# Kernel tuning notes

Measured on AMD Instinct MI355X. Metric: run time of the kernel, lower is better.

Reference implementation:

```python
import jax, jax.numpy as jnp
import numpy as np

KH, KW = 7, 7      # t2t kernel_size
ST = 3             # stride
PD = 3             # padding
K = KH * KW        # 49 taps per patch


def _patch_indices(H, W):
    """Linear indices into the padded (Hp,Wp) image for every (patch l, tap k)."""
    Hp, Wp = H + 2 * PD, W + 2 * PD
    oh = (H + 2 * PD - KH) // ST + 1
    ow = (W + 2 * PD - KW) // ST + 1
    ki, kj = np.meshgrid(np.arange(KH), np.arange(KW), indexing='ij')
    rows = (np.arange(oh) * ST)[:, None, None, None] + ki[None, None]   # (oh,1,kh,kw)
    cols = (np.arange(ow) * ST)[None, :, None, None] + kj[None, None]   # (1,ow,kh,kw)
    idx = (rows * Wp + cols).reshape(oh * ow, K)                        # (L, 49)
    return jnp.asarray(idx), Hp, Wp, oh * ow


def setup_inputs() -> dict:
    key = jax.random.key(0)
    k1, k2, k3 = jax.random.split(key, 3)
    b, n, d, hd = 2, 5760, 512, 1960
    return {
        'x': jax.random.normal(k1, (b, n, d), dtype=jnp.float32),
        'W1': jax.random.normal(k2, (d, hd), dtype=jnp.float32) * 0.02,
        'b1': jnp.zeros((hd,), dtype=jnp.float32),
        'W2': jax.random.normal(k3, (hd, d), dtype=jnp.float32) * 0.02,
        'b2': jnp.zeros((d,), dtype=jnp.float32),
        'out_h': 60,
        'out_w': 108,
    }


def reference(x, W1, b1, W2, b2, out_h, out_w):
    H, W = int(out_h), int(out_w)
    idx, Hp, Wp, L = _patch_indices(H, W)          # idx: (L, 49)
    idxf = idx.reshape(-1)                         # (L*49,)

    b, n, _ = x.shape
    h = x @ W1 + b1                                # (b, n, 1960)
    hd = h.shape[-1]
    C = hd // K                                    # 40 fold channels
    Bp = (b * n) // L                              # fold batch (= b * t)

    # fold input layout: (Bp, C, K, L) -> scatter-add into padded image
    patches = h.reshape(Bp, L, C, K)
    vals = jnp.transpose(patches, (0, 2, 1, 3)).reshape(Bp * C, L * K)
    img = jnp.zeros((Bp * C, Hp * Wp), x.dtype).at[:, idxf].add(vals)

    # overlap-count normalizer (fold of ones), same for every batch/channel
    count = jnp.zeros((Hp * Wp,), x.dtype).at[idxf].add(jnp.ones_like(idxf, x.dtype))

    # crop padding (as F.fold does), normalize, re-pad with zeros (as F.unfold does)
    img = img.reshape(Bp, C, Hp, Wp)[:, :, PD:PD + H, PD:PD + W]
    cnt = count.reshape(Hp, Wp)[PD:PD + H, PD:PD + W]
    img = img / cnt
    flat = jnp.pad(img, ((0, 0), (0, 0), (PD, PD), (PD, PD))).reshape(Bp * C, Hp * Wp)

    # unfold: gather the same taps back, restore (b, n, hd) token layout
    g = flat[:, idxf].reshape(Bp, C, L, K)
    g = jnp.transpose(g, (0, 2, 1, 3)).reshape(b, n, hd)

    return jax.nn.gelu(g, approximate=False) @ W2 + b2
```

## Files before the change

### kernel.cpp

```cpp
#include <hip/hip_runtime.h>

typedef _Float16 f16;
typedef __attribute__((ext_vector_type(8))) _Float16 half8;
typedef __attribute__((ext_vector_type(4))) _Float16 half4;
typedef __attribute__((ext_vector_type(4))) float f32x4;

#define LDS_AS __attribute__((address_space(3)))
#define GLB_AS __attribute__((address_space(1)))

__device__ __forceinline__ void load16_lds(const f16* g, f16* l) {
    __builtin_amdgcn_global_load_lds((GLB_AS void*)(g), (LDS_AS void*)(l), 16, 0, 0);
}

__global__ __launch_bounds__(256, 2) void gemm1(
    const f16* __restrict__ A, const f16* __restrict__ Bt,
    const float* __restrict__ bias, f16* __restrict__ C)
{
    const int id  = blockIdx.x;
    const int xcd = id & 7;
    const int r   = id >> 3;
    const int mt  = r & 15;
    const int nt  = xcd + 8 * (r >> 4);
    if (nt >= 90) return;
    const int m0 = mt * 128, n0 = nt * 128;
    const int K = 512, ldc = 11520;

    __shared__ f16 As[128 * 32];
    __shared__ f16 Bs[128 * 32];
    const int tid  = threadIdx.x;
    const int wave = tid >> 6;
    const int lane = tid & 63;

    const int s0 = tid, s1 = tid + 256;
    const f16* gA0 = A  + (m0 + (s0 >> 2)) * K + (s0 & 3) * 8;
    const f16* gA1 = A  + (m0 + (s1 >> 2)) * K + (s1 & 3) * 8;
    const f16* gB0 = Bt + (n0 + (s0 >> 2)) * K + (s0 & 3) * 8;
    const f16* gB1 = Bt + (n0 + (s1 >> 2)) * K + (s1 & 3) * 8;
    f16* lA0 = &As[wave * 512];
    f16* lA1 = &As[2048 + wave * 512];
    f16* lB0 = &Bs[wave * 512];
    f16* lB1 = &Bs[2048 + wave * 512];

    const int wm = (wave >> 1) * 64;
    const int wn = (wave & 1) * 64;
    const int lr = lane & 15;
    const int k8 = (lane >> 4) * 8;

    f32x4 acc[4][4];
#pragma unroll
    for (int i = 0; i < 4; ++i)
#pragma unroll
        for (int j = 0; j < 4; ++j) acc[i][j] = f32x4{0.f, 0.f, 0.f, 0.f};

    for (int k0 = 0; k0 < K; k0 += 32) {
        load16_lds(gA0 + k0, lA0);
        load16_lds(gA1 + k0, lA1);
        load16_lds(gB0 + k0, lB0);
        load16_lds(gB1 + k0, lB1);
        __syncthreads();
        half8 af[4], bf[4];
#pragma unroll
        for (int i = 0; i < 4; ++i)
            af[i] = *(const half8*)&As[(wm + i * 16 + lr) * 32 + k8];
#pragma unroll
        for (int j = 0; j < 4; ++j)
            bf[j] = *(const half8*)&Bs[(wn + j * 16 + lr) * 32 + k8];
#pragma unroll
        for (int i = 0; i < 4; ++i)
#pragma unroll
            for (int j = 0; j < 4; ++j)
                acc[i][j] = __builtin_amdgcn_mfma_f32_16x16x32_f16(
                    af[i], bf[j], acc[i][j], 0, 0, 0);
        __syncthreads();
    }

#pragma unroll
    for (int i = 0; i < 4; ++i) {
#pragma unroll
        for (int rr = 0; rr < 4; ++rr) {
            const int row = m0 + wm + i * 16 + (lane >> 4) * 4 + rr;
            const float bvr = (row < 1960) ? bias[row] : 0.f;
#pragma unroll
            for (int j = 0; j < 4; ++j) {
                const int col = n0 + wn + j * 16 + lr;
                C[row * ldc + col] = (f16)(acc[i][j][rr] + bvr);
            }
        }
    }
}

__global__ __launch_bounds__(256, 2) void gemm2(
    const f16* __restrict__ A, const f16* __restrict__ Bt,
    const float* __restrict__ bias, float* __restrict__ Cout)
{
    const int id  = blockIdx.x;
    const int xcd = id & 7;
    const int j2  = id >> 3;
    const int nt  = j2 & 3;
    const int mt  = (j2 >> 2) * 8 + xcd;
    if (mt >= 90) return;
    const int m0 = mt * 128, n0 = nt * 128;
    const int K = 2048;

    __shared__ f16 As[128 * 32];
    __shared__ f16 Bs[128 * 32];
    const int tid  = threadIdx.x;
    const int wave = tid >> 6;
    const int lane = tid & 63;

    const int s0 = tid, s1 = tid + 256;
    const f16* gA0 = A  + (m0 + (s0 >> 2)) * K + (s0 & 3) * 8;
    const f16* gA1 = A  + (m0 + (s1 >> 2)) * K + (s1 & 3) * 8;
    const f16* gB0 = Bt + (n0 + (s0 >> 2)) * K + (s0 & 3) * 8;
    const f16* gB1 = Bt + (n0 + (s1 >> 2)) * K + (s1 & 3) * 8;
    f16* lA0 = &As[wave * 512];
    f16* lA1 = &As[2048 + wave * 512];
    f16* lB0 = &Bs[wave * 512];
    f16* lB1 = &Bs[2048 + wave * 512];

    const int wm = (wave >> 1) * 64;
    const int wn = (wave & 1) * 64;
    const int lr = lane & 15;
    const int k8 = (lane >> 4) * 8;

    f32x4 acc[4][4];
#pragma unroll
    for (int i = 0; i < 4; ++i)
#pragma unroll
        for (int j = 0; j < 4; ++j) acc[i][j] = f32x4{0.f, 0.f, 0.f, 0.f};

    for (int k0 = 0; k0 < K; k0 += 32) {
        load16_lds(gA0 + k0, lA0);
        load16_lds(gA1 + k0, lA1);
        load16_lds(gB0 + k0, lB0);
        load16_lds(gB1 + k0, lB1);
        __syncthreads();
        half8 af[4], bf[4];
#pragma unroll
        for (int i = 0; i < 4; ++i)
            af[i] = *(const half8*)&As[(wm + i * 16 + lr) * 32 + k8];
#pragma unroll
        for (int j = 0; j < 4; ++j)
            bf[j] = *(const half8*)&Bs[(wn + j * 16 + lr) * 32 + k8];
#pragma unroll
        for (int i = 0; i < 4; ++i)
#pragma unroll
            for (int j = 0; j < 4; ++j)
                acc[i][j] = __builtin_amdgcn_mfma_f32_16x16x32_f16(
                    af[i], bf[j], acc[i][j], 0, 0, 0);
        __syncthreads();
    }

#pragma unroll
    for (int j = 0; j < 4; ++j) {
        const int col = n0 + wn + j * 16 + lr;
        const float bv = bias[col];
#pragma unroll
        for (int i = 0; i < 4; ++i) {
            const int rbase = m0 + wm + i * 16 + (lane >> 4) * 4;
#pragma unroll
            for (int rr = 0; rr < 4; ++rr)
                Cout[(rbase + rr) * 512 + col] = acc[i][j][rr] + bv;
        }
    }
}

__global__ void fold_gelu(const f16* __restrict__ h_t, f16* __restrict__ imgG)
{
    const int r  = blockIdx.x;
    const int bc = blockIdx.y;
    const int bp  = bc / 40;
    const int cch = bc % 40;
    const int c = threadIdx.x;
    if (c >= 114) return;
    float outv = 0.f;
    if (r >= 3 && r < 63 && c >= 3 && c < 111) {
        const int qr = r / 3, rm = r % 3;
        const int qc = c / 3, cm = c % 3;
        int kis[3], ohs[3], nr = 0;
        int kjs[3], ows[3], nc = 0;
#pragma unroll
        for (int t = 0; t < 3; ++t) {
            const int ki = rm + 3 * t, oh = qr - t;
            if (ki < 7 && oh >= 0 && oh < 20) { kis[nr] = ki; ohs[nr] = oh; ++nr; }
            const int kj = cm + 3 * t, ow = qc - t;
            if (kj < 7 && ow >= 0 && ow < 36) { kjs[nc] = kj; ows[nc] = ow; ++nc; }
        }
        float sum = 0.f;
        for (int a = 0; a < nr; ++a)
            for (int b = 0; b < nc; ++b) {
                const int n = cch * 49 + kis[a] * 7 + kjs[b];
                const int token = bp * 720 + ohs[a] * 36 + ows[b];
                sum += (float)h_t[n * 11520 + token];
            }
        const float xv = sum / (float)(nr * nc);
        outv = 0.5f * xv * (1.f + erff(xv * 0.70710678118654752f));
    }
    imgG[(bc * 66 + r) * 114 + c] = (f16)outv;
}

__global__ void unfold_g(const f16* __restrict__ imgG, f16* __restrict__ g16)
{
    const int i = blockIdx.x * 256 + threadIdx.x;
    const int t = i >> 11;
    const int j = i & 2047;
    f16 v = (f16)0.f;
    if (j < 1960) {
        const int bp = t / 720, l = t % 720;
        const int oh = l / 36, ow = l % 36;
        const int cch = j / 49, kk = j % 49;
        const int ki = kk / 7, kj = kk % 7;
        v = imgG[((bp * 40 + cch) * 66 + oh * 3 + ki) * 114 + ow * 3 + kj];
    }
    g16[i] = v;
}

__global__ void cvt_x(const float* __restrict__ x, f16* __restrict__ xh, int n4)
{
    const int i = blockIdx.x * 256 + threadIdx.x;
    if (i < n4) {
        const float4 v = ((const float4*)x)[i];
        half4 o;
        o[0] = (f16)v.x; o[1] = (f16)v.y; o[2] = (f16)v.z; o[3] = (f16)v.w;
        ((half4*)xh)[i] = o;
    }
}

__global__ void transpose_pad(const float* __restrict__ src, f16* __restrict__ dst,
                              int R, int C, int Rp, int Cp)
{
    __shared__ float tile[32][33];
    const int r0 = blockIdx.x * 32, c0 = blockIdx.y * 32;
    const int tx = threadIdx.x, ty = threadIdx.y;
#pragma unroll
    for (int i = 0; i < 32; i += 8) {
        const int r = r0 + ty + i, c = c0 + tx;
        tile[ty + i][tx] = (r < R && c < C) ? src[r * C + c] : 0.f;
    }
    __syncthreads();
#pragma unroll
    for (int i = 0; i < 32; i += 8) {
        const int c = c0 + ty + i, r = r0 + tx;
        if (c < Cp && r < Rp) dst[c * Rp + r] = (f16)tile[tx][ty + i];
    }
}

extern "C" void kernel_launch(void* const* d_in, const int* in_sizes, int n_in,
                              void* d_out, int out_size, void* d_ws, size_t ws_size,
                              hipStream_t stream)
{
    const float* x  = (const float*)d_in[0];
    const float* W1 = (const float*)d_in[1];
    const float* b1 = (const float*)d_in[2];
    const float* W2 = (const float*)d_in[3];
    const float* b2 = (const float*)d_in[4];

    char* ws = (char*)d_ws;
    f16* xh   = (f16*)(ws);
    f16* W1t  = (f16*)(ws + 11796480);
    f16* W2t  = (f16*)(ws + 11796480 + 2097152);
    f16* hbuf = (f16*)(ws + 11796480 + 2 * 2097152);
    f16* imgG = (f16*)(ws + 11796480 + 2 * 2097152 + 47185920);

    cvt_x<<<dim3(5760), dim3(256), 0, stream>>>(x, xh, 1474560);
    transpose_pad<<<dim3(16, 64), dim3(32, 8), 0, stream>>>(W1, W1t, 512, 1960, 512, 2048);
    transpose_pad<<<dim3(64, 16), dim3(32, 8), 0, stream>>>(W2, W2t, 1960, 512, 2048, 512);
    gemm1<<<dim3(1536), dim3(256), 0, stream>>>(W1t, xh, b1, hbuf);
    fold_gelu<<<dim3(66, 640), dim3(128), 0, stream>>>(hbuf, imgG);
    unfold_g<<<dim3(92160), dim3(256), 0, stream>>>(imgG, hbuf);
    gemm2<<<dim3(384), dim3(256), 0, stream>>>(hbuf, W2t, b2, (float*)d_out);
}
```

Before: 242.0 us.

## Double-buffer GEMM LDS loads, split-K gemm2 with atomics, LDS-staged unfold

Both GEMMs now use two LDS stages: the next K-slice is issued with global_load_lds before waiting on the current one (vmcnt(4) plus barrier), so memory latency overlaps MFMA work. gemm2 is split into two K halves across twice as many blocks. The halves accumulate with float atomicAdd into an output that a new bias_fill kernel pre-initializes. The unfold kernel now stages each channel image in LDS and writes the padded zero columns explicitly, avoiding one scattered global gather per element. The changes cost extra LDS, atomic traffic on the output and one additional kernel launch.

```diff
diff --git a/kernel.cpp b/kernel.cpp
--- a/kernel.cpp
+++ b/kernel.cpp
@@ -11,6 +11,10 @@
 __device__ __forceinline__ void load16_lds(const f16* g, f16* l) {
     __builtin_amdgcn_global_load_lds((GLB_AS void*)(g), (LDS_AS void*)(l), 16, 0, 0);
 }
+
+#define WAIT4_BARRIER()  asm volatile("s_waitcnt vmcnt(4)\n\ts_barrier" ::: "memory")
+#define WAIT0_BARRIER()  asm volatile("s_waitcnt vmcnt(0)\n\ts_barrier" ::: "memory")
+#define PLAIN_BARRIER()  asm volatile("s_barrier" ::: "memory")
 
 __global__ __launch_bounds__(256, 2) void gemm1(
     const f16* __restrict__ A, const f16* __restrict__ Bt,
@@ -25,8 +29,8 @@
     const int m0 = mt * 128, n0 = nt * 128;
     const int K = 512, ldc = 11520;
 
-    __shared__ f16 As[128 * 32];
-    __shared__ f16 Bs[128 * 32];
+    __shared__ f16 As[2][128 * 32];
+    __shared__ f16 Bs[2][128 * 32];
     const int tid  = threadIdx.x;
     const int wave = tid >> 6;
     const int lane = tid & 63;
@@ -36,10 +40,6 @@
     const f16* gA1 = A  + (m0 + (s1 >> 2)) * K + (s1 & 3) * 8;
     const f16* gB0 = Bt + (n0 + (s0 >> 2)) * K + (s0 & 3) * 8;
     const f16* gB1 = Bt + (n0 + (s1 >> 2)) * K + (s1 & 3) * 8;
-    f16* lA0 = &As[wave * 512];
-    f16* lA1 = &As[2048 + wave * 512];
-    f16* lB0 = &Bs[wave * 512];
-    f16* lB1 = &Bs[2048 + wave * 512];
 
     const int wm = (wave >> 1) * 64;
     const int wn = (wave & 1) * 64;
@@ -52,26 +52,37 @@
 #pragma unroll
         for (int j = 0; j < 4; ++j) acc[i][j] = f32x4{0.f, 0.f, 0.f, 0.f};
 
-    for (int k0 = 0; k0 < K; k0 += 32) {
-        load16_lds(gA0 + k0, lA0);
-        load16_lds(gA1 + k0, lA1);
-        load16_lds(gB0 + k0, lB0);
-        load16_lds(gB1 + k0, lB1);
-        __syncthreads();
+#define G1_ISSUE(st, k0) do { \
+    load16_lds(gA0 + (k0), &As[st][wave * 512]); \
+    load16_lds(gA1 + (k0), &As[st][2048 + wave * 512]); \
+    load16_lds(gB0 + (k0), &Bs[st][wave * 512]); \
+    load16_lds(gB1 + (k0), &Bs[st][2048 + wave * 512]); \
+} while (0)
+
+    G1_ISSUE(0, 0);
+    const int NS = 16;
+    for (int s = 0; s < NS; ++s) {
+        const int cur = s & 1;
+        if (s + 1 < NS) {
+            G1_ISSUE(cur ^ 1, (s + 1) * 32);
+            WAIT4_BARRIER();
+        } else {
+            WAIT0_BARRIER();
+        }
         half8 af[4], bf[4];
 #pragma unroll
         for (int i = 0; i < 4; ++i)
-            af[i] = *(const half8*)&As[(wm + i * 16 + lr) * 32 + k8];
+            af[i] = *(const half8*)&As[cur][(wm + i * 16 + lr) * 32 + k8];
 #pragma unroll
         for (int j = 0; j < 4; ++j)
-            bf[j] = *(const half8*)&Bs[(wn + j * 16 + lr) * 32 + k8];
+            bf[j] = *(const half8*)&Bs[cur][(wn + j * 16 + lr) * 32 + k8];
 #pragma unroll
         for (int i = 0; i < 4; ++i)
 #pragma unroll
             for (int j = 0; j < 4; ++j)
                 acc[i][j] = __builtin_amdgcn_mfma_f32_16x16x32_f16(
                     af[i], bf[j], acc[i][j], 0, 0, 0);
-        __syncthreads();
+        PLAIN_BARRIER();
     }
 
 #pragma unroll
@@ -91,32 +102,30 @@
 
 __global__ __launch_bounds__(256, 2) void gemm2(
     const f16* __restrict__ A, const f16* __restrict__ Bt,
-    const float* __restrict__ bias, float* __restrict__ Cout)
+    float* __restrict__ Cout)
 {
     const int id  = blockIdx.x;
     const int xcd = id & 7;
-    const int j2  = id >> 3;
-    const int nt  = j2 & 3;
-    const int mt  = (j2 >> 2) * 8 + xcd;
+    const int r   = id >> 3;
+    const int kh  = r & 1;
+    const int rr_ = r >> 1;
+    const int nt  = rr_ & 3;
+    const int mt  = (rr_ >> 2) * 8 + xcd;
     if (mt >= 90) return;
     const int m0 = mt * 128, n0 = nt * 128;
-    const int K = 2048;
-
-    __shared__ f16 As[128 * 32];
-    __shared__ f16 Bs[128 * 32];
+
+    __shared__ f16 As[2][128 * 32];
+    __shared__ f16 Bs[2][128 * 32];
     const int tid  = threadIdx.x;
     const int wave = tid >> 6;
     const int lane = tid & 63;
 
     const int s0 = tid, s1 = tid + 256;
-    const f16* gA0 = A  + (m0 + (s0 >> 2)) * K + (s0 & 3) * 8;
-    const f16* gA1 = A  + (m0 + (s1 >> 2)) * K + (s1 & 3) * 8;
-    const f16* gB0 = Bt + (n0 + (s0 >> 2)) * K + (s0 & 3) * 8;
-    const f16* gB1 = Bt + (n0 + (s1 >> 2)) * K + (s1 & 3) * 8;
-    f16* lA0 = &As[wave * 512];
-    f16* lA1 = &As[2048 + wave * 512];
-    f16* lB0 = &Bs[wave * 512];
-    f16* lB1 = &Bs[2048 + wave * 512];
+    const int kbase = kh * 1024;
+    const f16* gA0 = A  + (m0 + (s0 >> 2)) * 2048 + kbase + (s0 & 3) * 8;
+    const f16* gA1 = A  + (m0 + (s1 >> 2)) * 2048 + kbase + (s1 & 3) * 8;
+    const f16* gB0 = Bt + (n0 + (s0 >> 2)) * 2048 + kbase + (s0 & 3) * 8;
+    const f16* gB1 = Bt + (n0 + (s1 >> 2)) * 2048 + kbase + (s1 & 3) * 8;
 
     const int wm = (wave >> 1) * 64;
     const int wn = (wave & 1) * 64;
@@ -129,40 +138,56 @@
 #pragma unroll
         for (int j = 0; j < 4; ++j) acc[i][j] = f32x4{0.f, 0.f, 0.f, 0.f};
 
-    for (int k0 = 0; k0 < K; k0 += 32) {
-        load16_lds(gA0 + k0, lA0);
-        load16_lds(gA1 + k0, lA1);
-        load16_lds(gB0 + k0, lB0);
-        load16_lds(gB1 + k0, lB1);
-        __syncthreads();
+#define G2_ISSUE(st, k0) do { \
+    load16_lds(gA0 + (k0), &As[st][wave * 512]); \
+    load16_lds(gA1 + (k0), &As[st][2048 + wave * 512]); \
+    load16_lds(gB0 + (k0), &Bs[st][wave * 512]); \
+    load16_lds(gB1 + (k0), &Bs[st][2048 + wave * 512]); \
+} while (0)
+
+    G2_ISSUE(0, 0);
+    const int NS = 32;
+    for (int s = 0; s < NS; ++s) {
+        const int cur = s & 1;
+        if (s + 1 < NS) {
+            G2_ISSUE(cur ^ 1, (s + 1) * 32);
+            WAIT4_BARRIER();
+        } else {
+            WAIT0_BARRIER();
+        }
         half8 af[4], bf[4];
 #pragma unroll
         for (int i = 0; i < 4; ++i)
-            af[i] = *(const half8*)&As[(wm + i * 16 + lr) * 32 + k8];
+            af[i] = *(const half8*)&As[cur][(wm + i * 16 + lr) * 32 + k8];
 #pragma unroll
         for (int j = 0; j < 4; ++j)
-            bf[j] = *(const half8*)&Bs[(wn + j * 16 + lr) * 32 + k8];
+            bf[j] = *(const half8*)&Bs[cur][(wn + j * 16 + lr) * 32 + k8];
 #pragma unroll
         for (int i = 0; i < 4; ++i)
 #pragma unroll
             for (int j = 0; j < 4; ++j)
                 acc[i][j] = __builtin_amdgcn_mfma_f32_16x16x32_f16(
                     af[i], bf[j], acc[i][j], 0, 0, 0);
-        __syncthreads();
+        PLAIN_BARRIER();
     }
 
 #pragma unroll
     for (int j = 0; j < 4; ++j) {
         const int col = n0 + wn + j * 16 + lr;
-        const float bv = bias[col];
 #pragma unroll
         for (int i = 0; i < 4; ++i) {
             const int rbase = m0 + wm + i * 16 + (lane >> 4) * 4;
 #pragma unroll
-            for (int rr = 0; rr < 4; ++rr)
-                Cout[(rbase + rr) * 512 + col] = acc[i][j][rr] + bv;
-        }
-    }
+            for (int q = 0; q < 4; ++q)
+                atomicAdd(&Cout[(rbase + q) * 512 + col], acc[i][j][q]);
+        }
+    }
+}
+
+__global__ void bias_fill(const float* __restrict__ b2, float* __restrict__ out)
+{
+    const int i = blockIdx.x * 256 + threadIdx.x;
+    ((float4*)out)[i] = ((const float4*)b2)[i & 127];
 }
 
 __global__ void fold_gelu(const f16* __restrict__ h_t, f16* __restrict__ imgG)
@@ -199,20 +224,32 @@
     imgG[(bc * 66 + r) * 114 + c] = (f16)outv;
 }
 
-__global__ void unfold_g(const f16* __restrict__ imgG, f16* __restrict__ g16)
-{
-    const int i = blockIdx.x * 256 + threadIdx.x;
-    const int t = i >> 11;
-    const int j = i & 2047;
-    f16 v = (f16)0.f;
-    if (j < 1960) {
-        const int bp = t / 720, l = t % 720;
-        const int oh = l / 36, ow = l % 36;
-        const int cch = j / 49, kk = j % 49;
-        const int ki = kk / 7, kj = kk % 7;
-        v = imgG[((bp * 40 + cch) * 66 + oh * 3 + ki) * 114 + ow * 3 + kj];
-    }
-    g16[i] = v;
+__global__ __launch_bounds__(256) void unfold_lds(
+    const f16* __restrict__ imgG, f16* __restrict__ g16)
+{
+    __shared__ f16 ch[7524];
+    const int bc = blockIdx.x;
+    const int bp = bc / 40, cch = bc % 40;
+    const float* src = (const float*)(imgG + bc * 7524);
+    float* dst = (float*)ch;
+    for (int i = threadIdx.x; i < 3762; i += 256) dst[i] = src[i];
+    __syncthreads();
+    const int tokbase = bp * 720;
+    const int colbase = cch * 49;
+    for (int flat = threadIdx.x; flat < 35280; flat += 256) {
+        const int l = flat / 49, k = flat - l * 49;
+        const int oh = l / 36, ow = l - oh * 36;
+        const int ki = k / 7,  kj = k - ki * 7;
+        g16[(tokbase + l) * 2048 + colbase + k] =
+            ch[(oh * 3 + ki) * 114 + ow * 3 + kj];
+    }
+    if (cch >= 36) {
+        const int cb = 1960 + (cch - 36) * 22;
+        for (int flat = threadIdx.x; flat < 720 * 22; flat += 256) {
+            const int l = flat / 22, k = flat - l * 22;
+            g16[(tokbase + l) * 2048 + cb + k] = (f16)0.f;
+        }
+    }
 }
 
 __global__ void cvt_x(const float* __restrict__ x, f16* __restrict__ xh, int n4)
@@ -267,6 +304,7 @@
     transpose_pad<<<dim3(64, 16), dim3(32, 8), 0, stream>>>(W2, W2t, 1960, 512, 2048, 512);
     gemm1<<<dim3(1536), dim3(256), 0, stream>>>(W1t, xh, b1, hbuf);
     fold_gelu<<<dim3(66, 640), dim3(128), 0, stream>>>(hbuf, imgG);
-    unfold_g<<<dim3(92160), dim3(256), 0, stream>>>(imgG, hbuf);
-    gemm2<<<dim3(384), dim3(256), 0, stream>>>(hbuf, W2t, b2, (float*)d_out);
-}
+    unfold_lds<<<dim3(640), dim3(256), 0, stream>>>(imgG, hbuf);
+    bias_fill<<<dim3(5760), dim3(256), 0, stream>>>(b2, (float*)d_out);
+    gemm2<<<dim3(768), dim3(256), 0, stream>>>(hbuf, W2t, (float*)d_out);
+}
```

After: 258.0 us. +6.6%, slower.
